# Kernel optimization log

Hardware: AMD Instinct MI355X
Metric: run time of the kernel (lower is better)

## Reference

```python
import jax, jax.numpy as jnp
import numpy as np

N, L = 4096, 512

def setup_inputs() -> dict:
    key = jax.random.key(0)
    ks = jax.random.split(key, 12)
    def w(k, shape, fan_in):
        return jax.random.normal(k, shape, jnp.float32) / np.sqrt(fan_in)
    inp = {
        'samples': jax.random.normal(ks[0], (N, 1, L), jnp.float32),
        'samples_info': jax.random.randint(ks[1], (N, 2), 0, 2).astype(jnp.int64),
        'conv1_w': w(ks[2], (64, 1, 100), 100),
        'conv1_b': jnp.zeros((64,), jnp.float32),
        'conv2_w': w(ks[3], (128, 64, 5), 64 * 5),
        'conv2_b': jnp.zeros((128,), jnp.float32),
        'conv3_w': w(ks[4], (256, 128, 3), 128 * 3),
        'conv3_b': jnp.zeros((256,), jnp.float32),
        'fc_w': w(ks[5], (128, 256), 256),
        'fc_b': jnp.zeros((128,), jnp.float32),
        'bn_gamma': jnp.ones((128,), jnp.float32),
        'bn_beta': jnp.zeros((128,), jnp.float32),
        'bn_mean': jnp.zeros((128,), jnp.float32),
        'bn_var': jnp.ones((128,), jnp.float32),
    }
    return inp

def _conv1d(x, w, b, pad):
    # x: [N,C,L], w: [O,C,K]; torch padding='same' for k=100 pads (49,50)
    y = jax.lax.conv_general_dilated(x, w, window_strides=(1,), padding=[pad],
                                     dimension_numbers=('NCH', 'OIH', 'NCH'))
    return y + b[None, :, None]

def _maxpool2(x):
    n, c, l = x.shape
    return x.reshape(n, c, l // 2, 2).max(-1)

def reference(samples, samples_info, conv1_w, conv1_b, conv2_w, conv2_b,
              conv3_w, conv3_b, fc_w, fc_b, bn_gamma, bn_beta, bn_mean, bn_var):
    h = _maxpool2(jax.nn.relu(_conv1d(samples, conv1_w, conv1_b, (49, 50))))
    h = _maxpool2(jax.nn.relu(_conv1d(h, conv2_w, conv2_b, (2, 2))))
    h = _maxpool2(jax.nn.relu(_conv1d(h, conv3_w, conv3_b, (1, 1))))
    h = h.mean(-1)                                  # AdaptiveAvgPool1d(1)+Flatten -> [N,256]
    h = jax.nn.relu(h @ fc_w.T + fc_b)              # Linear 256->128
    z = bn_gamma * (h - bn_mean) * jax.lax.rsqrt(bn_var + 1e-5) + bn_beta  # BN (eval)
    # all-pairs euclidean distances via the cdist identity (replaces N^2 python loop)
    sq = jnp.sum(z * z, axis=-1)
    d2 = sq[:, None] + sq[None, :] - 2.0 * (z @ z.T)
    n = z.shape[0]
    offdiag = ~jnp.eye(n, dtype=bool)
    d = jnp.sqrt(jnp.where(offdiag, jnp.maximum(d2, 0.0), 1.0))
    writer = samples_info[:, 0]
    gen = samples_info[:, 1]
    y = ((writer[:, None] == writer[None, :]) & (gen[:, None] == 1) & (gen[None, :] == 1)).astype(z.dtype)
    cl = jnp.where(offdiag, y * d + (1.0 - y) * jax.nn.relu(1.0 - d), 0.0)
    return cl  # [N,N] contrastive loss per ordered pair (i!=j); diagonal masked to 0
```

## Files before the change

### kernel.cpp

```cpp
#include <hip/hip_runtime.h>
#include <math.h>

#define NS 4096

typedef _Float16 half8 __attribute__((ext_vector_type(8)));
typedef _Float16 half2v __attribute__((ext_vector_type(2)));
typedef float floatx16 __attribute__((ext_vector_type(16)));

#define P1T_OFF     0
#define P1T_STRIDE  72
#define P2T_OFF     9360
#define P2T_STRIDE  136
#define XC_OFF      9360
#define XC_STRIDE   648
#define SCR_OFF     1024
#define B1_OFF      18200
#define B2_OFF      18264
#define B3_OFF      18392
#define PR_OFF      18648
#define LDS_MAIN_FLOATS 19288

__global__ void prep_weights(const float* __restrict__ w1,
                             const float* __restrict__ w2,
                             const float* __restrict__ w3,
                             _Float16* __restrict__ w1p,
                             _Float16* __restrict__ w2p,
                             _Float16* __restrict__ w3p)
{
    int gid = blockIdx.x * 256 + threadIdx.x;
    if (gid < 8192) {
        int m = gid >> 7, k = gid & 127;
        w1p[gid] = (k < 100) ? (_Float16)w1[m * 100 + k] : (_Float16)0.f;
    } else if (gid < 49152) {
        int r = gid - 8192;
        int dk = r >> 13, rem = r & 8191;
        int m = rem >> 6, i = rem & 63;
        w2p[r] = (_Float16)w2[(m * 64 + i) * 5 + dk];
    } else if (gid < 147456) {
        int r = gid - 49152;
        int dk = r >> 15, rem = r & 32767;
        int m = rem >> 7, i = rem & 127;
        w3p[r] = (_Float16)w3[(m * 128 + i) * 3 + dk];
    }
}

__device__ __forceinline__ float dpp_rowsum16(float v) {
    int x;
    x = __builtin_amdgcn_update_dpp(0, __float_as_int(v), 0x111, 0xF, 0xF, true);
    v += __int_as_float(x);
    x = __builtin_amdgcn_update_dpp(0, __float_as_int(v), 0x112, 0xF, 0xF, true);
    v += __int_as_float(x);
    x = __builtin_amdgcn_update_dpp(0, __float_as_int(v), 0x114, 0xF, 0xF, true);
    v += __int_as_float(x);
    x = __builtin_amdgcn_update_dpp(0, __float_as_int(v), 0x118, 0xF, 0xF, true);
    v += __int_as_float(x);
    return v;
}


__global__ __launch_bounds__(512, 4)
void cnn_fused(const float* __restrict__ samples, const int* __restrict__ info,
               const _Float16* __restrict__ w1p,
               const _Float16* __restrict__ w2p,
               const _Float16* __restrict__ w3p,
               const float* __restrict__ b1, const float* __restrict__ b2,
               const float* __restrict__ b3,
               const float* __restrict__ fcw, const float* __restrict__ fcb,
               const float* __restrict__ gamma_, const float* __restrict__ beta_,
               const float* __restrict__ bnm, const float* __restrict__ bnv,
               _Float16* __restrict__ zh, float* __restrict__ sqout,
               int* __restrict__ uout)
{
    extern __shared__ float lds[];
    _Float16* p1T = (_Float16*)(lds + P1T_OFF);
    _Float16* p2T = (_Float16*)(lds + P2T_OFF);
    _Float16* xc  = (_Float16*)(lds + XC_OFF);

    const int n    = blockIdx.x;
    const int t    = threadIdx.x;
    const int lane = t & 63;
    const int wave = t >> 6;
    const int g    = lane >> 5;
    const int col  = lane & 31;

    {
        const float* sp = samples + n * 512;
        const int c = wave;
        for (int u = lane; u < XC_STRIDE; u += 64) {
            int src = u + c - 49;
            xc[c * XC_STRIDE + u] = (_Float16)((src >= 0 && src < 512) ? sp[src] : 0.f);
        }
    }
    if (t < 64)              lds[B1_OFF + t] = b1[t];
    if (t >= 64 && t < 192)  lds[B2_OFF + (t - 64)] = b2[t - 64];
    if (t >= 192 && t < 448) lds[B3_OFF + (t - 192)] = b3[t - 192];
    for (int i = t; i < 640; i += 512) {
        int k = i & 127;
        const float* p = (i < 128) ? fcb : (i < 256) ? gamma_ : (i < 384) ? beta_
                       : (i < 512) ? bnm : bnv;
        lds[PR_OFF + i] = p[k];
    }
    if (t < 144) {
        int rr = t / 36, c4 = t - rr * 36;
        int row = (rr < 2) ? rr : (256 + rr);
        lds[P1T_OFF + row * 36 + c4] = 0.f;
    }
    if (t == 0) uout[n] = (info[2 * n + 1] == 1) ? info[2 * n] : -1;
    __syncthreads();

    auto pool_store = [&](floatx16& acc, _Float16* dst) {
        float vm[16];
        #pragma unroll
        for (int r = 0; r < 16; ++r) {
            float v = fmaxf(acc[r], 0.f);
            vm[r] = fmaxf(v, __shfl_xor(v, 1));
        }
        if (!(lane & 1)) {
            #pragma unroll
            for (int rq = 0; rq < 4; ++rq) {
                half2v p0, p1;
                p0[0] = (_Float16)vm[4 * rq];     p0[1] = (_Float16)vm[4 * rq + 1];
                p1[0] = (_Float16)vm[4 * rq + 2]; p1[1] = (_Float16)vm[4 * rq + 3];
                *(half2v*)(dst + 8 * rq)     = p0;
                *(half2v*)(dst + 8 * rq + 2) = p1;
            }
        }
    };

    {
        const int mt   = wave >> 2;
        const int ntb1 = (wave & 3) * 4;
        const _Float16* ap = w1p + (mt * 32 + col) * 128 + g * 8;
        const _Float16* bps[4];
        #pragma unroll
        for (int s = 0; s < 4; ++s) {
            const int nt = ntb1 + s;
            const int nn = nt * 32 + col;
            const int c  = nn & 7;
            bps[s] = xc + c * XC_STRIDE + (nn - c) + g * 8;
        }
        floatx16 acc[4];
        #pragma unroll
        for (int q4 = 0; q4 < 4; ++q4) {
            float4 bq = *(const float4*)&lds[B1_OFF + mt * 32 + 8 * q4 + 4 * g];
            #pragma unroll
            for (int s = 0; s < 4; ++s) {
                acc[s][4 * q4 + 0] = bq.x; acc[s][4 * q4 + 1] = bq.y;
                acc[s][4 * q4 + 2] = bq.z; acc[s][4 * q4 + 3] = bq.w;
            }
        }
        half8 Aa[3], Bb[2][4];
        Aa[0] = *(const half8*)(ap);
        Aa[1] = *(const half8*)(ap + 16);
        #pragma unroll
        for (int s = 0; s < 4; ++s) Bb[0][s] = *(const half8*)(bps[s]);
        #pragma unroll
        for (int i = 0; i < 7; ++i) {
            if (i < 5)
                Aa[(i + 2) % 3] = *(const half8*)(ap + (i + 2) * 16);
            if (i < 6) {
                #pragma unroll
                for (int s = 0; s < 4; ++s)
                    Bb[(i + 1) & 1][s] = *(const half8*)(bps[s] + (i + 1) * 16);
            }
            #pragma unroll
            for (int s = 0; s < 4; ++s)
                acc[s] = __builtin_amdgcn_mfma_f32_32x32x16_f16(Aa[i % 3], Bb[i & 1][s], acc[s], 0, 0, 0);
        }
        #pragma unroll
        for (int s = 0; s < 4; ++s) {
            const int P = 2 + (ntb1 + s) * 16 + (col >> 1);
            pool_store(acc[s], p1T + P * P1T_STRIDE + mt * 32 + 4 * g);
        }
    }
    __syncthreads();

    {
        if (t < 136) {
            int row = (t < 68) ? 0 : 129;
            int c4 = (t < 68) ? t : (t - 68);
            lds[P2T_OFF + row * 68 + c4] = 0.f;
        }
        const int mt  = wave & 3;
        const int ntb = (wave >> 2) * 4;
        const _Float16* ap = w2p + (mt * 32 + col) * 64 + g * 8;
        const _Float16* bps[4];
        #pragma unroll
        for (int s = 0; s < 4; ++s)
            bps[s] = p1T + ((ntb + s) * 32 + col) * P1T_STRIDE + g * 8;
        floatx16 acc[4];
        #pragma unroll
        for (int q4 = 0; q4 < 4; ++q4) {
            float4 bq = *(const float4*)&lds[B2_OFF + mt * 32 + 8 * q4 + 4 * g];
            #pragma unroll
            for (int s = 0; s < 4; ++s) {
                acc[s][4 * q4 + 0] = bq.x; acc[s][4 * q4 + 1] = bq.y;
                acc[s][4 * q4 + 2] = bq.z; acc[s][4 * q4 + 3] = bq.w;
            }
        }
        half8 Aa[3], Bb[2][4];
        Aa[0] = *(const half8*)(ap);
        Aa[1] = *(const half8*)(ap + 16);
        #pragma unroll
        for (int s = 0; s < 4; ++s) Bb[0][s] = *(const half8*)(bps[s]);
        #pragma unroll
        for (int i = 0; i < 20; ++i) {
            if (i < 18) {
                const int j = i + 2, dkj = j >> 2, kbj = j & 3;
                Aa[(i + 2) % 3] = *(const half8*)(ap + dkj * 8192 + kbj * 16);
            }
            if (i < 19) {
                const int j = i + 1, dkj = j >> 2, kbj = j & 3;
                #pragma unroll
                for (int s = 0; s < 4; ++s)
                    Bb[j & 1][s] = *(const half8*)(bps[s] + dkj * P1T_STRIDE + kbj * 16);
            }
            #pragma unroll
            for (int s = 0; s < 4; ++s)
                acc[s] = __builtin_amdgcn_mfma_f32_32x32x16_f16(Aa[i % 3], Bb[i & 1][s], acc[s], 0, 0, 0);
        }
        #pragma unroll
        for (int s = 0; s < 4; ++s) {
            const int P = 1 + (ntb + s) * 16 + (col >> 1);
            pool_store(acc[s], p2T + P * P2T_STRIDE + mt * 32 + 4 * g);
        }
    }
    __syncthreads();

    {
        const int mt = wave;
        const _Float16* ap = w3p + (mt * 32 + col) * 128 + g * 8;
        const _Float16* bps[4];
        #pragma unroll
        for (int s = 0; s < 4; ++s)
            bps[s] = p2T + (s * 32 + col) * P2T_STRIDE + g * 8;
        floatx16 acc[4];
        #pragma unroll
        for (int q4 = 0; q4 < 4; ++q4) {
            float4 bq = *(const float4*)&lds[B3_OFF + mt * 32 + 8 * q4 + 4 * g];
            #pragma unroll
            for (int s = 0; s < 4; ++s) {
                acc[s][4 * q4 + 0] = bq.x; acc[s][4 * q4 + 1] = bq.y;
                acc[s][4 * q4 + 2] = bq.z; acc[s][4 * q4 + 3] = bq.w;
            }
        }
        half8 Aa[3], Bb[2][4];
        Aa[0] = *(const half8*)(ap);
        Aa[1] = *(const half8*)(ap + 16);
        #pragma unroll
        for (int s = 0; s < 4; ++s) Bb[0][s] = *(const half8*)(bps[s]);
        #pragma unroll
        for (int i = 0; i < 24; ++i) {
            if (i < 22) {
                const int j = i + 2, dkj = j >> 3, kbj = j & 7;
                Aa[(i + 2) % 3] = *(const half8*)(ap + dkj * 32768 + kbj * 16);
            }
            if (i < 23) {
                const int j = i + 1, dkj = j >> 3, kbj = j & 7;
                #pragma unroll
                for (int s = 0; s < 4; ++s)
                    Bb[j & 1][s] = *(const half8*)(bps[s] + dkj * P2T_STRIDE + kbj * 16);
            }
            #pragma unroll
            for (int s = 0; s < 4; ++s)
                acc[s] = __builtin_amdgcn_mfma_f32_32x32x16_f16(Aa[i % 3], Bb[i & 1][s], acc[s], 0, 0, 0);
        }
        #pragma unroll
        for (int r = 0; r < 16; ++r) {
            float srow = 0.f;
            #pragma unroll
            for (int s = 0; s < 4; ++s) {
                float v = fmaxf(acc[s][r], 0.f);
                srow += fmaxf(v, __shfl_xor(v, 1));
            }
            float s16 = dpp_rowsum16(srow);
            float s32 = s16 + __shfl_xor(s16, 16);
            if ((lane & 31) == 15) {
                int ch = mt * 32 + (r & 3) + 8 * (r >> 2) + 4 * g;
                lds[SCR_OFF + ch] = s32 * (1.f / 128.f);
            }
        }
    }
    __syncthreads();

    {
        const float4 xv = *(const float4*)&lds[SCR_OFF + 4 * lane];
        float sqpart = 0.f;
        #pragma unroll 1
        for (int ow = 0; ow < 16; ow += 4) {
            const int o0 = wave * 16 + ow;
            const float4 w0 = *(const float4*)&fcw[(o0 + 0) * 256 + 4 * lane];
            const float4 w1 = *(const float4*)&fcw[(o0 + 1) * 256 + 4 * lane];
            const float4 w2 = *(const float4*)&fcw[(o0 + 2) * 256 + 4 * lane];
            const float4 w3 = *(const float4*)&fcw[(o0 + 3) * 256 + 4 * lane];
            float s0 = w0.x * xv.x + w0.y * xv.y + w0.z * xv.z + w0.w * xv.w;
            float s1 = w1.x * xv.x + w1.y * xv.y + w1.z * xv.z + w1.w * xv.w;
            float s2 = w2.x * xv.x + w2.y * xv.y + w2.z * xv.z + w2.w * xv.w;
            float s3 = w3.x * xv.x + w3.y * xv.y + w3.z * xv.z + w3.w * xv.w;
            #pragma unroll
            for (int off = 32; off > 0; off >>= 1) {
                s0 += __shfl_down(s0, off);
                s1 += __shfl_down(s1, off);
                s2 += __shfl_down(s2, off);
                s3 += __shfl_down(s3, off);
            }
            if (lane == 0) {
                float sv[4] = {s0, s1, s2, s3};
                half2v zp0, zp1;
                #pragma unroll
                for (int k = 0; k < 4; ++k) {
                    float hv = fmaxf(sv[k] + lds[PR_OFF + o0 + k], 0.f);
                    float zv = lds[PR_OFF + 128 + o0 + k] * (hv - lds[PR_OFF + 384 + o0 + k])
                             * (1.f / sqrtf(lds[PR_OFF + 512 + o0 + k] + 1e-5f))
                             + lds[PR_OFF + 256 + o0 + k];
                    _Float16 zq = (_Float16)zv;
                    if (k < 2) zp0[k] = zq; else zp1[k - 2] = zq;
                    float zqf = (float)zq;
                    sqpart += zqf * zqf;
                }
                *(half2v*)(zh + (size_t)n * 128 + o0)     = zp0;
                *(half2v*)(zh + (size_t)n * 128 + o0 + 2) = zp1;
            }
        }
        if (lane == 0) lds[SCR_OFF + 256 + wave] = sqpart;
    }
    __syncthreads();
    if (t == 0) {
        float s = 0.f;
        #pragma unroll
        for (int w = 0; w < 8; ++w) s += lds[SCR_OFF + 256 + w];
        sqout[n] = s;
    }
}

#define PW_STRIDE 136
#define PW_LDS_BYTES (128 * PW_STRIDE * 2)

__global__ __launch_bounds__(256, 4)
void pairwise_mfma(const _Float16* __restrict__ zh, const float* __restrict__ sq,
                   const int* __restrict__ u, float* __restrict__ out)
{
    extern __shared__ float ldsf[];
    _Float16* bt = (_Float16*)ldsf;
    const int t = threadIdx.x;
    const int i0 = blockIdx.y * 128;
    const int j0 = blockIdx.x * 128;

    #pragma unroll
    for (int r4 = 0; r4 < 8; ++r4) {
        int idx = t + 256 * r4;
        int row = idx >> 4, c8 = (idx & 15) * 8;
        *(half8*)(bt + row * PW_STRIDE + c8) = *(const half8*)(zh + (size_t)(j0 + row) * 128 + c8);
    }
    __syncthreads();

    const int lane = t & 63, wave = t >> 6;
    const int g = lane >> 5, col = lane & 31;
    const int ib = (wave & 1) * 64, jb = (wave >> 1) * 64;

    const _Float16* ap0 = zh + (size_t)(i0 + ib + col) * 128 + g * 8;
    const _Float16* ap1 = zh + (size_t)(i0 + ib + 32 + col) * 128 + g * 8;
    const _Float16* bp0 = bt + (jb + col) * PW_STRIDE + g * 8;
    const _Float16* bp1 = bt + (jb + 32 + col) * PW_STRIDE + g * 8;

    floatx16 acc[2][2];
    #pragma unroll
    for (int a = 0; a < 2; ++a)
        #pragma unroll
        for (int b = 0; b < 2; ++b)
            #pragma unroll
            for (int r = 0; r < 16; ++r) acc[a][b][r] = 0.f;

    half8 A0[2], A1[2], B0[2], B1[2];
    A0[0] = *(const half8*)(ap0);
    A1[0] = *(const half8*)(ap1);
    B0[0] = *(const half8*)(bp0);
    B1[0] = *(const half8*)(bp1);
    #pragma unroll
    for (int kb = 0; kb < 8; ++kb) {
        if (kb < 7) {
            A0[(kb + 1) & 1] = *(const half8*)(ap0 + (kb + 1) * 16);
            A1[(kb + 1) & 1] = *(const half8*)(ap1 + (kb + 1) * 16);
            B0[(kb + 1) & 1] = *(const half8*)(bp0 + (kb + 1) * 16);
            B1[(kb + 1) & 1] = *(const half8*)(bp1 + (kb + 1) * 16);
        }
        acc[0][0] = __builtin_amdgcn_mfma_f32_32x32x16_f16(A0[kb & 1], B0[kb & 1], acc[0][0], 0, 0, 0);
        acc[0][1] = __builtin_amdgcn_mfma_f32_32x32x16_f16(A0[kb & 1], B1[kb & 1], acc[0][1], 0, 0, 0);
        acc[1][0] = __builtin_amdgcn_mfma_f32_32x32x16_f16(A1[kb & 1], B0[kb & 1], acc[1][0], 0, 0, 0);
        acc[1][1] = __builtin_amdgcn_mfma_f32_32x32x16_f16(A1[kb & 1], B1[kb & 1], acc[1][1], 0, 0, 0);
    }

    #pragma unroll
    for (int nt = 0; nt < 2; ++nt) {
        const int j = j0 + jb + nt * 32 + col;
        const float sqj = sq[j];
        const int uj = u[j];
        #pragma unroll
        for (int mt = 0; mt < 2; ++mt) {
            #pragma unroll
            for (int r = 0; r < 16; ++r) {
                const int i = i0 + ib + mt * 32 + (r & 3) + 8 * (r >> 2) + 4 * g;
                float res;
                if (i == j) {
                    res = 0.f;
                } else {
                    float d2 = sq[i] + sqj - 2.f * acc[mt][nt][r];
                    float d = sqrtf(fmaxf(d2, 0.f));
                    int ui = u[i];
                    res = (ui == uj && ui >= 0) ? d : fmaxf(1.f - d, 0.f);
                }
                out[(size_t)i * 4096 + j] = res;
            }
        }
    }
}

extern "C" void kernel_launch(void* const* d_in, const int* in_sizes, int n_in,
                              void* d_out, int out_size, void* d_ws, size_t ws_size,
                              hipStream_t stream)
{
    const float* samples = (const float*)d_in[0];
    const int*   info    = (const int*)d_in[1];
    const float* w1  = (const float*)d_in[2];
    const float* b1  = (const float*)d_in[3];
    const float* w2  = (const float*)d_in[4];
    const float* b2  = (const float*)d_in[5];
    const float* w3  = (const float*)d_in[6];
    const float* b3  = (const float*)d_in[7];
    const float* fcw = (const float*)d_in[8];
    const float* fcb = (const float*)d_in[9];
    const float* g   = (const float*)d_in[10];
    const float* be  = (const float*)d_in[11];
    const float* bm  = (const float*)d_in[12];
    const float* bv  = (const float*)d_in[13];
    float* out = (float*)d_out;

    _Float16* zhws = (_Float16*)d_ws;
    float*    sqws = (float*)((char*)d_ws + (1 << 20));
    int*      uws  = (int*)((char*)d_ws + (1 << 20) + 16384);
    _Float16* wp   = (_Float16*)((char*)d_ws + (1 << 20) + 32768);
    _Float16* w1p = wp;
    _Float16* w2p = wp + 8192;
    _Float16* w3p = wp + 49152;

    hipLaunchKernelGGL(prep_weights, dim3(576), dim3(256), 0, stream,
                       w1, w2, w3, w1p, w2p, w3p);

    hipLaunchKernelGGL(cnn_fused, dim3(NS), dim3(512),
                       LDS_MAIN_FLOATS * sizeof(float), stream,
                       samples, info, w1p, w2p, w3p, b1, b2, b3, fcw, fcb,
                       g, be, bm, bv, zhws, sqws, uws);

    hipLaunchKernelGGL(pairwise_mfma, dim3(32, 32), dim3(256),
                       PW_LDS_BYTES, stream,
                       zhws, sqws, uws, out);
}
```

Measured before the change: 428.1 us.

## Prefetch weights across barriers, raise MFMA priority, stage pairwise A tile in LDS

The first conv weight fragments for each conv stage are now loaded before the preceding barrier, and the fc weights are loaded before their barrier and double-buffered, so global-load latency overlaps with synchronization. MFMA blocks are wrapped in s_setprio to favor matrix issue. In the pairwise kernel, the A rows now go through LDS alongside B and are held entirely in registers. The B loop is reordered so each B fragment feeds two MFMAs. This doubles the LDS footprint and lowers launch bounds from 4 to 2 blocks per CU, which may reduce occupancy.

Measured after the change: 424.8 us. Within noise of the previous version (-0.8%).

```diff
diff --git a/kernel.cpp b/kernel.cpp
--- a/kernel.cpp
+++ b/kernel.cpp
@@ -106,6 +106,11 @@
         lds[P1T_OFF + row * 36 + c4] = 0.f;
     }
     if (t == 0) uout[n] = (info[2 * n + 1] == 1) ? info[2 * n] : -1;
+
+    const int mt1 = wave >> 2;
+    const _Float16* ap1 = w1p + (mt1 * 32 + col) * 128 + g * 8;
+    half8 a1_0 = *(const half8*)(ap1);
+    half8 a1_1 = *(const half8*)(ap1 + 16);
     __syncthreads();
 
     auto pool_store = [&](floatx16& acc, _Float16* dst) {
@@ -128,9 +133,9 @@
     };
 
     {
-        const int mt   = wave >> 2;
+        const int mt   = mt1;
         const int ntb1 = (wave & 3) * 4;
-        const _Float16* ap = w1p + (mt * 32 + col) * 128 + g * 8;
+        const _Float16* ap = ap1;
         const _Float16* bps[4];
         #pragma unroll
         for (int s = 0; s < 4; ++s) {
@@ -150,8 +155,8 @@
             }
         }
         half8 Aa[3], Bb[2][4];
-        Aa[0] = *(const half8*)(ap);
-        Aa[1] = *(const half8*)(ap + 16);
+        Aa[0] = a1_0;
+        Aa[1] = a1_1;
         #pragma unroll
         for (int s = 0; s < 4; ++s) Bb[0][s] = *(const half8*)(bps[s]);
         #pragma unroll
@@ -163,9 +168,11 @@
                 for (int s = 0; s < 4; ++s)
                     Bb[(i + 1) & 1][s] = *(const half8*)(bps[s] + (i + 1) * 16);
             }
+            __builtin_amdgcn_s_setprio(1);
             #pragma unroll
             for (int s = 0; s < 4; ++s)
                 acc[s] = __builtin_amdgcn_mfma_f32_32x32x16_f16(Aa[i % 3], Bb[i & 1][s], acc[s], 0, 0, 0);
+            __builtin_amdgcn_s_setprio(0);
         }
         #pragma unroll
         for (int s = 0; s < 4; ++s) {
@@ -173,6 +180,10 @@
             pool_store(acc[s], p1T + P * P1T_STRIDE + mt * 32 + 4 * g);
         }
     }
+    const int mt2 = wave & 3;
+    const _Float16* ap2 = w2p + (mt2 * 32 + col) * 64 + g * 8;
+    half8 a2_0 = *(const half8*)(ap2);
+    half8 a2_1 = *(const half8*)(ap2 + 16);
     __syncthreads();
 
     {
@@ -181,9 +192,9 @@
             int c4 = (t < 68) ? t : (t - 68);
             lds[P2T_OFF + row * 68 + c4] = 0.f;
         }
-        const int mt  = wave & 3;
+        const int mt  = mt2;
         const int ntb = (wave >> 2) * 4;
-        const _Float16* ap = w2p + (mt * 32 + col) * 64 + g * 8;
+        const _Float16* ap = ap2;
         const _Float16* bps[4];
         #pragma unroll
         for (int s = 0; s < 4; ++s)
@@ -199,8 +210,8 @@
             }
         }
         half8 Aa[3], Bb[2][4];
-        Aa[0] = *(const half8*)(ap);
-        Aa[1] = *(const half8*)(ap + 16);
+        Aa[0] = a2_0;
+        Aa[1] = a2_1;
         #pragma unroll
         for (int s = 0; s < 4; ++s) Bb[0][s] = *(const half8*)(bps[s]);
         #pragma unroll
@@ -215,9 +226,11 @@
                 for (int s = 0; s < 4; ++s)
                     Bb[j & 1][s] = *(const half8*)(bps[s] + dkj * P1T_STRIDE + kbj * 16);
             }
+            __builtin_amdgcn_s_setprio(1);
             #pragma unroll
             for (int s = 0; s < 4; ++s)
                 acc[s] = __builtin_amdgcn_mfma_f32_32x32x16_f16(Aa[i % 3], Bb[i & 1][s], acc[s], 0, 0, 0);
+            __builtin_amdgcn_s_setprio(0);
         }
         #pragma unroll
         for (int s = 0; s < 4; ++s) {
@@ -225,11 +238,14 @@
             pool_store(acc[s], p2T + P * P2T_STRIDE + mt * 32 + 4 * g);
         }
     }
+    const _Float16* ap3 = w3p + (wave * 32 + col) * 128 + g * 8;
+    half8 a3_0 = *(const half8*)(ap3);
+    half8 a3_1 = *(const half8*)(ap3 + 16);
     __syncthreads();
 
     {
         const int mt = wave;
-        const _Float16* ap = w3p + (mt * 32 + col) * 128 + g * 8;
+        const _Float16* ap = ap3;
         const _Float16* bps[4];
         #pragma unroll
         for (int s = 0; s < 4; ++s)
@@ -245,8 +261,8 @@
             }
         }
         half8 Aa[3], Bb[2][4];
-        Aa[0] = *(const half8*)(ap);
-        Aa[1] = *(const half8*)(ap + 16);
+        Aa[0] = a3_0;
+        Aa[1] = a3_1;
         #pragma unroll
         for (int s = 0; s < 4; ++s) Bb[0][s] = *(const half8*)(bps[s]);
         #pragma unroll
@@ -261,9 +277,11 @@
                 for (int s = 0; s < 4; ++s)
                     Bb[j & 1][s] = *(const half8*)(bps[s] + dkj * P2T_STRIDE + kbj * 16);
             }
+            __builtin_amdgcn_s_setprio(1);
             #pragma unroll
             for (int s = 0; s < 4; ++s)
                 acc[s] = __builtin_amdgcn_mfma_f32_32x32x16_f16(Aa[i % 3], Bb[i & 1][s], acc[s], 0, 0, 0);
+            __builtin_amdgcn_s_setprio(0);
         }
         #pragma unroll
         for (int r = 0; r < 16; ++r) {
@@ -281,22 +299,31 @@
             }
         }
     }
+    float4 Wc[4];
+    {
+        const int o0p = wave * 16;
+        #pragma unroll
+        for (int k = 0; k < 4; ++k)
+            Wc[k] = *(const float4*)&fcw[(o0p + k) * 256 + 4 * lane];
+    }
     __syncthreads();
 
     {
         const float4 xv = *(const float4*)&lds[SCR_OFF + 4 * lane];
         float sqpart = 0.f;
-        #pragma unroll 1
-        for (int ow = 0; ow < 16; ow += 4) {
-            const int o0 = wave * 16 + ow;
-            const float4 w0 = *(const float4*)&fcw[(o0 + 0) * 256 + 4 * lane];
-            const float4 w1 = *(const float4*)&fcw[(o0 + 1) * 256 + 4 * lane];
-            const float4 w2 = *(const float4*)&fcw[(o0 + 2) * 256 + 4 * lane];
-            const float4 w3 = *(const float4*)&fcw[(o0 + 3) * 256 + 4 * lane];
-            float s0 = w0.x * xv.x + w0.y * xv.y + w0.z * xv.z + w0.w * xv.w;
-            float s1 = w1.x * xv.x + w1.y * xv.y + w1.z * xv.z + w1.w * xv.w;
-            float s2 = w2.x * xv.x + w2.y * xv.y + w2.z * xv.z + w2.w * xv.w;
-            float s3 = w3.x * xv.x + w3.y * xv.y + w3.z * xv.z + w3.w * xv.w;
+        #pragma unroll
+        for (int j = 0; j < 4; ++j) {
+            const int o0 = wave * 16 + j * 4;
+            float4 Wn[4];
+            if (j < 3) {
+                #pragma unroll
+                for (int k = 0; k < 4; ++k)
+                    Wn[k] = *(const float4*)&fcw[(o0 + 4 + k) * 256 + 4 * lane];
+            }
+            float s0 = Wc[0].x * xv.x + Wc[0].y * xv.y + Wc[0].z * xv.z + Wc[0].w * xv.w;
+            float s1 = Wc[1].x * xv.x + Wc[1].y * xv.y + Wc[1].z * xv.z + Wc[1].w * xv.w;
+            float s2 = Wc[2].x * xv.x + Wc[2].y * xv.y + Wc[2].z * xv.z + Wc[2].w * xv.w;
+            float s3 = Wc[3].x * xv.x + Wc[3].y * xv.y + Wc[3].z * xv.z + Wc[3].w * xv.w;
             #pragma unroll
             for (int off = 32; off > 0; off >>= 1) {
                 s0 += __shfl_down(s0, off);
@@ -321,6 +348,10 @@
                 *(half2v*)(zh + (size_t)n * 128 + o0)     = zp0;
                 *(half2v*)(zh + (size_t)n * 128 + o0 + 2) = zp1;
             }
+            if (j < 3) {
+                #pragma unroll
+                for (int k = 0; k < 4; ++k) Wc[k] = Wn[k];
+            }
         }
         if (lane == 0) lds[SCR_OFF + 256 + wave] = sqpart;
     }
@@ -334,14 +365,15 @@
 }
 
 #define PW_STRIDE 136
-#define PW_LDS_BYTES (128 * PW_STRIDE * 2)
-
-__global__ __launch_bounds__(256, 4)
+#define PW_LDS_BYTES (2 * 128 * PW_STRIDE * 2)
+
+__global__ __launch_bounds__(256, 2)
 void pairwise_mfma(const _Float16* __restrict__ zh, const float* __restrict__ sq,
                    const int* __restrict__ u, float* __restrict__ out)
 {
     extern __shared__ float ldsf[];
-    _Float16* bt = (_Float16*)ldsf;
+    _Float16* at = (_Float16*)ldsf;
+    _Float16* bt = at + 128 * PW_STRIDE;
     const int t = threadIdx.x;
     const int i0 = blockIdx.y * 128;
     const int j0 = blockIdx.x * 128;
@@ -350,6 +382,7 @@
     for (int r4 = 0; r4 < 8; ++r4) {
         int idx = t + 256 * r4;
         int row = idx >> 4, c8 = (idx & 15) * 8;
+        *(half8*)(at + row * PW_STRIDE + c8) = *(const half8*)(zh + (size_t)(i0 + row) * 128 + c8);
         *(half8*)(bt + row * PW_STRIDE + c8) = *(const half8*)(zh + (size_t)(j0 + row) * 128 + c8);
     }
     __syncthreads();
@@ -358,10 +391,12 @@
     const int g = lane >> 5, col = lane & 31;
     const int ib = (wave & 1) * 64, jb = (wave >> 1) * 64;
 
-    const _Float16* ap0 = zh + (size_t)(i0 + ib + col) * 128 + g * 8;
-    const _Float16* ap1 = zh + (size_t)(i0 + ib + 32 + col) * 128 + g * 8;
-    const _Float16* bp0 = bt + (jb + col) * PW_STRIDE + g * 8;
-    const _Float16* bp1 = bt + (jb + 32 + col) * PW_STRIDE + g * 8;
+    half8 A[2][8];
+    #pragma unroll
+    for (int mt = 0; mt < 2; ++mt)
+        #pragma unroll
+        for (int kb = 0; kb < 8; ++kb)
+            A[mt][kb] = *(const half8*)(at + (ib + mt * 32 + col) * PW_STRIDE + kb * 16 + g * 8);
 
     floatx16 acc[2][2];
     #pragma unroll
@@ -371,24 +406,16 @@
             #pragma unroll
             for (int r = 0; r < 16; ++r) acc[a][b][r] = 0.f;
 
-    half8 A0[2], A1[2], B0[2], B1[2];
-    A0[0] = *(const half8*)(ap0);
-    A1[0] = *(const half8*)(ap1);
-    B0[0] = *(const half8*)(bp0);
-    B1[0] = *(const half8*)(bp1);
+    __builtin_amdgcn_s_setprio(1);
     #pragma unroll
-    for (int kb = 0; kb < 8; ++kb) {
-        if (kb < 7) {
-            A0[(kb + 1) & 1] = *(const half8*)(ap0 + (kb + 1) * 16);
-            A1[(kb + 1) & 1] = *(const half8*)(ap1 + (kb + 1) * 16);
-            B0[(kb + 1) & 1] = *(const half8*)(bp0 + (kb + 1) * 16);
-            B1[(kb + 1) & 1] = *(const half8*)(bp1 + (kb + 1) * 16);
-        }
-        acc[0][0] = __builtin_amdgcn_mfma_f32_32x32x16_f16(A0[kb & 1], B0[kb & 1], acc[0][0], 0, 0, 0);
-        acc[0][1] = __builtin_amdgcn_mfma_f32_32x32x16_f16(A0[kb & 1], B1[kb & 1], acc[0][1], 0, 0, 0);
-        acc[1][0] = __builtin_amdgcn_mfma_f32_32x32x16_f16(A1[kb & 1], B0[kb & 1], acc[1][0], 0, 0, 0);
-        acc[1][1] = __builtin_amdgcn_mfma_f32_32x32x16_f16(A1[kb & 1], B1[kb & 1], acc[1][1], 0, 0, 0);
-    }
+    for (int nt = 0; nt < 2; ++nt)
+        #pragma unroll
+        for (int kb = 0; kb < 8; ++kb) {
+            half8 B = *(const half8*)(bt + (jb + nt * 32 + col) * PW_STRIDE + kb * 16 + g * 8);
+            acc[0][nt] = __builtin_amdgcn_mfma_f32_32x32x16_f16(A[0][kb], B, acc[0][nt], 0, 0, 0);
+            acc[1][nt] = __builtin_amdgcn_mfma_f32_32x32x16_f16(A[1][kb], B, acc[1][nt], 0, 0, 0);
+        }
+    __builtin_amdgcn_s_setprio(0);
 
     #pragma unroll
     for (int nt = 0; nt < 2; ++nt) {
```
